# Kernel optimization log

Hardware: AMD Instinct MI355X
Metric: run time of the kernel (lower is better)

## Reference

```python
import jax, jax.numpy as jnp
import numpy as np

N = 50000
E = 800000
IN_DIM = 128
HID = 64
HEADS = 4
NUM_CLASSES = 40
NEG_SLOPE = 0.2
BN_EPS = 1e-5
SM_EPS = 1e-16


def setup_inputs() -> dict:
    key = jax.random.key(0)
    ks = jax.random.split(key, 12)
    d1 = HID * HEADS
    s_in = 1.0 / np.sqrt(IN_DIM)
    s_d1 = 1.0 / np.sqrt(d1)
    return {
        "x": jax.random.normal(ks[0], (N, IN_DIM), dtype=jnp.float32),
        "edge_index": jax.random.randint(ks[1], (2, E), 0, N, dtype=jnp.int32),
        # layer 1 (heads=4, concat)
        "Wl1": jax.random.normal(ks[2], (IN_DIM, d1), dtype=jnp.float32) * s_in,
        "Wr1": jax.random.normal(ks[3], (IN_DIM, d1), dtype=jnp.float32) * s_in,
        "att1": jax.random.normal(ks[4], (HEADS, HID), dtype=jnp.float32) * (1.0 / np.sqrt(HID)),
        "b1": jnp.zeros((d1,), dtype=jnp.float32),
        "gamma1": jnp.ones((d1,), dtype=jnp.float32),
        "beta1": jnp.zeros((d1,), dtype=jnp.float32),
        # layer 2 (heads=1, mean)
        "Wl2": jax.random.normal(ks[5], (d1, NUM_CLASSES), dtype=jnp.float32) * s_d1,
        "Wr2": jax.random.normal(ks[6], (d1, NUM_CLASSES), dtype=jnp.float32) * s_d1,
        "att2": jax.random.normal(ks[7], (1, NUM_CLASSES), dtype=jnp.float32) * (1.0 / np.sqrt(NUM_CLASSES)),
        "b2": jnp.zeros((NUM_CLASSES,), dtype=jnp.float32),
    }


def _gatv2_conv(x, Wl, Wr, att, b, src, dst, heads, out_ch, concat):
    n = x.shape[0]
    xl = (x @ Wl).reshape(n, heads, out_ch)   # source transform
    xr = (x @ Wr).reshape(n, heads, out_ch)   # target transform
    # per-edge attention logits (GATv2): a^T LeakyReLU(xl_j + xr_i)
    s = xl[src] + xr[dst]                                    # [E, H, C]
    e = jnp.einsum('ehc,hc->eh', jax.nn.leaky_relu(s, NEG_SLOPE), att)  # [E, H]
    # segment softmax over incoming edges of each dst node
    m = jax.ops.segment_max(e, dst, num_segments=n)          # [N, H]
    a = jnp.exp(e - m[dst])
    denom = jax.ops.segment_sum(a, dst, num_segments=n)
    alpha = a / (denom[dst] + SM_EPS)                        # [E, H]
    # aggregate messages alpha * xl_j
    out = jax.ops.segment_sum(alpha[..., None] * xl[src], dst, num_segments=n)  # [N, H, C]
    out = out.reshape(n, heads * out_ch) if concat else out.mean(axis=1)
    return out + b


def _batchnorm(h, gamma, beta):
    mu = h.mean(axis=0)
    var = h.var(axis=0)
    return gamma * (h - mu) * jax.lax.rsqrt(var + BN_EPS) + beta


def reference(x, edge_index, Wl1, Wr1, att1, b1, gamma1, beta1, Wl2, Wr2, att2, b2):
    n = x.shape[0]
    # add self-loops (PyG GATv2Conv default add_self_loops=True)
    loop = jnp.arange(n, dtype=edge_index.dtype)
    src = jnp.concatenate([edge_index[0], loop])
    dst = jnp.concatenate([edge_index[1], loop])
    h = _gatv2_conv(x, Wl1, Wr1, att1, b1, src, dst, HEADS, HID, True)
    h = jax.nn.elu(_batchnorm(h, gamma1, beta1))
    # eval mode: dropout is identity
    return _gatv2_conv(h, Wl2, Wr2, att2, b2, src, dst, 1, NUM_CLASSES, False)
```

## Files before the change

kernel.cpp:

```cpp
#include <hip/hip_runtime.h>
#include <math.h>

#define N_NODES 50000
#define N_EDGES 800000
#define ET (N_EDGES + N_NODES)
#define IN_DIM 128
#define HID 64
#define HEADS 4
#define D1 256
#define NCLS 40
#define NEG_SLOPE 0.2f
#define BN_EPS 1e-5f
#define SM_EPS 1e-16f
#define NB 196

typedef unsigned short ushort_t;
typedef __attribute__((ext_vector_type(8))) short short8;
typedef __attribute__((ext_vector_type(16))) float f32x16;

__device__ __forceinline__ float eluf(float x) { return x > 0.f ? x : expm1f(x); }
__device__ __forceinline__ float lrelu(float x) { return x >= 0.f ? x : NEG_SLOPE * x; }
__device__ __forceinline__ unsigned short f2bf(float f) {
    unsigned int u = __float_as_uint(f);
    u += 0x7fffu + ((u >> 16) & 1u);
    return (unsigned short)(u >> 16);
}
__device__ __forceinline__ float bf2f(ushort_t u) {
    return __uint_as_float(((unsigned int)u) << 16);
}

__global__ void k_deg(const int* __restrict__ ei, int* __restrict__ deg) {
    int e = blockIdx.x * blockDim.x + threadIdx.x;
    if (e >= ET) return;
    int dst = (e < N_EDGES) ? ei[N_EDGES + e] : (e - N_EDGES);
    atomicAdd(&deg[dst], 1);
}

__global__ __launch_bounds__(256) void k_scan1(const int* __restrict__ deg,
                                               int* __restrict__ row_st,
                                               int* __restrict__ bsum) {
    __shared__ int wsum[4], woff[4];
    const int t = threadIdx.x, w = t >> 6, lane = t & 63;
    const int idx = blockIdx.x * 256 + t;
    int v = (idx < N_NODES) ? deg[idx] : 0;
    int s = v;
    #pragma unroll
    for (int off = 1; off < 64; off <<= 1) {
        int y = __shfl_up(s, off, 64);
        if (lane >= off) s += y;
    }
    if (lane == 63) wsum[w] = s;
    __syncthreads();
    if (t == 0) {
        int run = 0;
        #pragma unroll
        for (int i2 = 0; i2 < 4; i2++) { woff[i2] = run; run += wsum[i2]; }
        bsum[blockIdx.x] = run;
    }
    __syncthreads();
    if (idx < N_NODES) row_st[idx] = woff[w] + (s - v);
}

__global__ __launch_bounds__(256) void k_scan2(int* __restrict__ bsum) {
    __shared__ int wsum[4], woff[4];
    const int t = threadIdx.x, w = t >> 6, lane = t & 63;
    int v = (t < NB) ? bsum[t] : 0;
    int s = v;
    #pragma unroll
    for (int off = 1; off < 64; off <<= 1) {
        int y = __shfl_up(s, off, 64);
        if (lane >= off) s += y;
    }
    if (lane == 63) wsum[w] = s;
    __syncthreads();
    if (t == 0) {
        int run = 0;
        #pragma unroll
        for (int i2 = 0; i2 < 4; i2++) { woff[i2] = run; run += wsum[i2]; }
    }
    __syncthreads();
    if (t < NB) bsum[t] = woff[w] + (s - v);
}

__global__ void k_scan3(int* __restrict__ row_st, int* __restrict__ cursor,
                        const int* __restrict__ bsum) {
    const int idx = blockIdx.x * 256 + threadIdx.x;
    if (idx < N_NODES) {
        int r = row_st[idx] + bsum[blockIdx.x];
        row_st[idx] = r;
        cursor[idx] = r;
    }
    if (idx == 0) row_st[N_NODES] = ET;
}

__global__ void k_scatter(const int* __restrict__ ei, int* __restrict__ cursor,
                          int* __restrict__ csr_src) {
    int e = blockIdx.x * blockDim.x + threadIdx.x;
    if (e >= ET) return;
    int src, dst;
    if (e < N_EDGES) { src = ei[e]; dst = ei[N_EDGES + e]; }
    else             { src = dst = e - N_EDGES; }
    int pos = atomicAdd(&cursor[dst], 1);
    csr_src[pos] = src;
}

__global__ void k_cvt_x(const float* __restrict__ x, ushort_t* __restrict__ xb, int n4) {
    int i = blockIdx.x * blockDim.x + threadIdx.x;
    if (i >= n4) return;
    float4 v = ((const float4*)x)[i];
    ushort4 o;
    o.x = f2bf(v.x); o.y = f2bf(v.y); o.z = f2bf(v.z); o.w = f2bf(v.w);
    ((ushort4*)xb)[i] = o;
}

__global__ void k_cvt_w1(const float* __restrict__ Wl, const float* __restrict__ Wr,
                         ushort_t* __restrict__ BT) {
    int n = blockIdx.x;
    int k = threadIdx.x;
    float v = (n < 256) ? Wl[k * 256 + n] : Wr[k * 256 + (n - 256)];
    BT[n * 128 + k] = f2bf(v);
}

__global__ void k_cvt_w2(const float* __restrict__ Wl, const float* __restrict__ Wr,
                         ushort_t* __restrict__ BT) {
    int n = blockIdx.x;
    int k = threadIdx.x;
    float v = 0.f;
    if (n < 40)      v = Wl[k * 40 + n];
    else if (n < 80) v = Wr[k * 40 + (n - 40)];
    BT[n * 256 + k] = f2bf(v);
}

__global__ void k_cvt_h(const float* __restrict__ h1, const float* __restrict__ g,
                        const float* __restrict__ b, ushort_t* __restrict__ h1b) {
    int i = blockIdx.x * blockDim.x + threadIdx.x;
    int c0 = (threadIdx.x * 4) & 255;
    float4 v = ((const float4*)h1)[i];
    ushort4 o;
    o.x = f2bf(eluf(g[c0 + 0] * v.x + b[c0 + 0]));
    o.y = f2bf(eluf(g[c0 + 1] * v.y + b[c0 + 1]));
    o.z = f2bf(eluf(g[c0 + 2] * v.z + b[c0 + 2]));
    o.w = f2bf(eluf(g[c0 + 3] * v.w + b[c0 + 3]));
    ((ushort4*)h1b)[i] = o;
}

#define MBM 128
#define MBN 128
#define MBK 64
template<typename OT>
__global__ __launch_bounds__(256) void k_mgemm(
    const ushort_t* __restrict__ A, const ushort_t* __restrict__ BT,
    OT* __restrict__ C, int M, int K, int N, int ldc)
{
    __shared__ __align__(16) ushort_t Al[MBM * MBK];
    __shared__ __align__(16) ushort_t Bl[MBN * MBK];
    const int t = threadIdx.x;
    const int w = t >> 6, L = t & 63;
    const int i0 = blockIdx.x * MBM;
    const int j0 = blockIdx.y * MBN;
    const int wm = (w >> 1) * 64, wn = (w & 1) * 64;
    const int l31 = L & 31, half = L >> 5;

    int sm[4], sca[4];
    #pragma unroll
    for (int r = 0; r < 4; r++) {
        int s = (r * 4 + w) * 64 + L;
        int m = s >> 3;
        sm[r] = m;
        sca[r] = (s & 7) ^ (m & 7);
    }

    f32x16 acc[2][2];
    #pragma unroll
    for (int a = 0; a < 2; a++)
        #pragma unroll
        for (int b = 0; b < 2; b++)
            #pragma unroll
            for (int r = 0; r < 16; r++) acc[a][b][r] = 0.f;

    for (int kt = 0; kt < K; kt += MBK) {
        short8 sa[4], sb[4];
        #pragma unroll
        for (int r = 0; r < 4; r++) {
            int row = i0 + sm[r]; if (row >= M) row = M - 1;
            sa[r] = *(const short8*)&A[(size_t)row * K + kt + sca[r] * 8];
            sb[r] = *(const short8*)&BT[(size_t)(j0 + sm[r]) * K + kt + sca[r] * 8];
        }
        __syncthreads();
        #pragma unroll
        for (int r = 0; r < 4; r++) {
            int s = (r * 4 + w) * 64 + L;
            *(short8*)&Al[s * 8] = sa[r];
            *(short8*)&Bl[s * 8] = sb[r];
        }
        __syncthreads();
        #pragma unroll
        for (int ks = 0; ks < 4; ks++) {
            short8 af[2], bfr[2];
            #pragma unroll
            for (int mt = 0; mt < 2; mt++) {
                int m = wm + mt * 32 + l31;
                int c = (ks * 2 + half) ^ (m & 7);
                af[mt] = *(const short8*)&Al[(m * 8 + c) * 8];
            }
            #pragma unroll
            for (int nt = 0; nt < 2; nt++) {
                int n = wn + nt * 32 + l31;
                int c = (ks * 2 + half) ^ (n & 7);
                bfr[nt] = *(const short8*)&Bl[(n * 8 + c) * 8];
            }
            #pragma unroll
            for (int mt = 0; mt < 2; mt++)
                #pragma unroll
                for (int nt = 0; nt < 2; nt++)
                    acc[mt][nt] = __builtin_amdgcn_mfma_f32_32x32x16_bf16(
                        af[mt], bfr[nt], acc[mt][nt], 0, 0, 0);
        }
    }
    #pragma unroll
    for (int mt = 0; mt < 2; mt++)
        #pragma unroll
        for (int nt = 0; nt < 2; nt++) {
            int col = j0 + wn + nt * 32 + l31;
            int rbase = i0 + wm + mt * 32 + 4 * half;
            if (col < N) {
                #pragma unroll
                for (int r = 0; r < 16; r++) {
                    int row = rbase + (r & 3) + 8 * (r >> 2);
                    if (row < M) {
                        if constexpr (sizeof(OT) == 2)
                            C[(size_t)row * ldc + col] = (OT)f2bf(acc[mt][nt][r]);
                        else
                            C[(size_t)row * ldc + col] = acc[mt][nt][r];
                    }
                }
            }
        }
}

#define CH1 16
#define XLS 260
__global__ __launch_bounds__(256) void k_node1(
    const ushort_t* __restrict__ xlr, const int* __restrict__ row_start,
    const int* __restrict__ csr_src, const float* __restrict__ att1,
    const float* __restrict__ b1, float* __restrict__ h1)
{
    __shared__ __align__(16) float xl_sh[CH1 * XLS];
    __shared__ __align__(16) float xr_sh[D1];
    __shared__ __align__(16) float att_sh[D1];
    __shared__ __align__(16) float p_sh[HEADS][CH1];
    __shared__ int src_sh[CH1];
    const int i = blockIdx.x;
    const int t = threadIdx.x;
    const int h = t >> 6, lane = t & 63;
    const int qe = lane >> 2, qq = lane & 3;
    const int half = lane >> 5, l31 = lane & 31;
    const int s0 = row_start[i], s1 = row_start[i + 1];
    xr_sh[t] = bf2f(xlr[(size_t)i * 512 + 256 + t]);
    att_sh[t] = att1[t];
    const float bvv = b1[t];
    __syncthreads();

    float xr_t[16], at_t[16];
    {
        const float* xrp = &xr_sh[h * 64 + qq * 16];
        const float* atp = &att_sh[h * 64 + qq * 16];
        #pragma unroll
        for (int k = 0; k < 16; k += 4) {
            float4 a = *(const float4*)&xrp[k];
            float4 b = *(const float4*)&atp[k];
            xr_t[k + 0] = a.x; xr_t[k + 1] = a.y; xr_t[k + 2] = a.z; xr_t[k + 3] = a.w;
            at_t[k + 0] = b.x; at_t[k + 1] = b.y; at_t[k + 2] = b.z; at_t[k + 3] = b.w;
        }
    }

    float acc = 0.f, l_run = 0.f;

    int base = s0;
    const int nfull = (s1 - s0) >> 4;
    for (int f = 0; f < nfull; f++, base += CH1) {
        __syncthreads();
        if (t < CH1) src_sh[t] = csr_src[base + t];
        __syncthreads();
        #pragma unroll
        for (int r = 0; r < 2; r++) {
            int e = r * 8 + h * 2 + half;
            const ushort_t* gp = &xlr[(size_t)src_sh[e] * 512];
            ushort4 u0 = *(const ushort4*)&gp[4 * l31];
            ushort4 u1 = *(const ushort4*)&gp[128 + 4 * l31];
            float4 f0 = make_float4(bf2f(u0.x), bf2f(u0.y), bf2f(u0.z), bf2f(u0.w));
            float4 f1 = make_float4(bf2f(u1.x), bf2f(u1.y), bf2f(u1.z), bf2f(u1.w));
            *(float4*)&xl_sh[e * XLS + 4 * l31] = f0;
            *(float4*)&xl_sh[e * XLS + 128 + 4 * l31] = f1;
        }
        __syncthreads();
        float dot = 0.f;
        {
            const float* xp = &xl_sh[qe * XLS + h * 64 + qq * 16];
            #pragma unroll
            for (int k = 0; k < 16; k += 4) {
                float4 v = *(const float4*)&xp[k];
                dot += lrelu(v.x + xr_t[k + 0]) * at_t[k + 0];
                dot += lrelu(v.y + xr_t[k + 1]) * at_t[k + 1];
                dot += lrelu(v.z + xr_t[k + 2]) * at_t[k + 2];
                dot += lrelu(v.w + xr_t[k + 3]) * at_t[k + 3];
            }
        }
        dot += __shfl_xor(dot, 1, 64);
        dot += __shfl_xor(dot, 2, 64);
        if (qq == 0) p_sh[h][qe] = __expf(dot);
        float4 P0 = *(const float4*)&p_sh[h][0];
        float4 P1 = *(const float4*)&p_sh[h][4];
        float4 P2 = *(const float4*)&p_sh[h][8];
        float4 P3 = *(const float4*)&p_sh[h][12];
        float p[16] = {P0.x, P0.y, P0.z, P0.w, P1.x, P1.y, P1.z, P1.w,
                       P2.x, P2.y, P2.z, P2.w, P3.x, P3.y, P3.z, P3.w};
        float lsum = 0.f;
        #pragma unroll
        for (int e = 0; e < 16; e++) lsum += p[e];
        l_run += lsum;
        #pragma unroll
        for (int e = 0; e < 16; e++)
            acc += p[e] * xl_sh[e * XLS + t];
    }
    const int rem = s1 - base;
    if (rem > 0) {
        __syncthreads();
        if (t < rem) src_sh[t] = csr_src[base + t];
        __syncthreads();
        #pragma unroll
        for (int r = 0; r < 2; r++) {
            int e = r * 8 + h * 2 + half;
            if (e < rem) {
                const ushort_t* gp = &xlr[(size_t)src_sh[e] * 512];
                ushort4 u0 = *(const ushort4*)&gp[4 * l31];
                ushort4 u1 = *(const ushort4*)&gp[128 + 4 * l31];
                float4 f0 = make_float4(bf2f(u0.x), bf2f(u0.y), bf2f(u0.z), bf2f(u0.w));
                float4 f1 = make_float4(bf2f(u1.x), bf2f(u1.y), bf2f(u1.z), bf2f(u1.w));
                *(float4*)&xl_sh[e * XLS + 4 * l31] = f0;
                *(float4*)&xl_sh[e * XLS + 128 + 4 * l31] = f1;
            }
        }
        __syncthreads();
        float dot = 0.f;
        {
            const float* xp = &xl_sh[qe * XLS + h * 64 + qq * 16];
            #pragma unroll
            for (int k = 0; k < 16; k += 4) {
                float4 v = *(const float4*)&xp[k];
                dot += lrelu(v.x + xr_t[k + 0]) * at_t[k + 0];
                dot += lrelu(v.y + xr_t[k + 1]) * at_t[k + 1];
                dot += lrelu(v.z + xr_t[k + 2]) * at_t[k + 2];
                dot += lrelu(v.w + xr_t[k + 3]) * at_t[k + 3];
            }
        }
        dot += __shfl_xor(dot, 1, 64);
        dot += __shfl_xor(dot, 2, 64);
        if (qq == 0) p_sh[h][qe] = (qe < rem) ? __expf(dot) : 0.f;
        for (int e = 0; e < rem; e++) {
            float pe = p_sh[h][e];
            l_run += pe;
            acc += pe * xl_sh[e * XLS + t];
        }
    }
    h1[(size_t)i * 256 + t] = acc / (l_run + SM_EPS) + bvv;
}

__global__ void k_bnstats(const float* __restrict__ h1, float* __restrict__ bn_sum,
                          float* __restrict__ bn_sumsq) {
    const int t = threadIdx.x;
    const int rows_per = (N_NODES + gridDim.x - 1) / gridDim.x;
    const int r0 = blockIdx.x * rows_per;
    const int r1 = min(N_NODES, r0 + rows_per);
    float s = 0.f, s2 = 0.f;
    for (int r = r0; r < r1; r++) {
        float v = h1[(size_t)r * 256 + t];
        s += v; s2 += v * v;
    }
    atomicAdd(&bn_sum[t], s);
    atomicAdd(&bn_sumsq[t], s2);
}

__global__ void k_bnfinal(const float* __restrict__ bn_sum, const float* __restrict__ bn_sumsq,
                          const float* __restrict__ gamma, const float* __restrict__ beta,
                          float* __restrict__ bn_g, float* __restrict__ bn_b) {
    const int t = threadIdx.x;
    float mean = bn_sum[t] * (1.f / N_NODES);
    float var = bn_sumsq[t] * (1.f / N_NODES) - mean * mean;
    float g = gamma[t] * rsqrtf(var + BN_EPS);
    bn_g[t] = g;
    bn_b[t] = beta[t] - g * mean;
}

#define C2S 44
__global__ __launch_bounds__(256) void k_node2(
    const ushort_t* __restrict__ xlr2, const int* __restrict__ row_start,
    const int* __restrict__ csr_src, const float* __restrict__ att2,
    const float* __restrict__ b2, float* __restrict__ out)
{
    __shared__ __align__(16) float xl_sh[4][16 * C2S];
    __shared__ __align__(16) float p_sh[4][16];
    __shared__ float xr_blk[4][NCLS];
    __shared__ int src_sh[4][16];
    const int wv = threadIdx.x >> 6, L = threadIdx.x & 63;
    const int i = blockIdx.x * 4 + wv;
    const int qe = L >> 2, qq = L & 3;
    const bool node_ok = (i < N_NODES);
    int s0 = 0, s1 = 0;
    if (node_ok) { s0 = row_start[i]; s1 = row_start[i + 1]; }
    if (node_ok && L < NCLS) xr_blk[wv][L] = bf2f(xlr2[(size_t)i * 80 + 40 + L]);
    float at_t[10], xr_t[10];
    #pragma unroll
    for (int r = 0; r < 10; r++) at_t[r] = att2[qq + 4 * r];
    if (node_ok) {
        #pragma unroll
        for (int r = 0; r < 10; r++) xr_t[r] = xr_blk[wv][qq + 4 * r];
    }

    float accv = 0.f, l_run = 0.f;
    const int cagg = (L < NCLS) ? L : 0;

    if (node_ok)
    for (int base = s0; base < s1; base += 16) {
        const int cnt = min(16, s1 - base);
        if (L < cnt) src_sh[wv][L] = csr_src[base + L];
        {
            int e = L & 15, k = L >> 4;
            float4 f0 = make_float4(0.f, 0.f, 0.f, 0.f), f1 = f0;
            if (e < cnt) {
                short8 u = *(const short8*)&xlr2[(size_t)src_sh[wv][e] * 80 + k * 8];
                f0 = make_float4(bf2f((ushort_t)u[0]), bf2f((ushort_t)u[1]),
                                 bf2f((ushort_t)u[2]), bf2f((ushort_t)u[3]));
                f1 = make_float4(bf2f((ushort_t)u[4]), bf2f((ushort_t)u[5]),
                                 bf2f((ushort_t)u[6]), bf2f((ushort_t)u[7]));
            }
            *(float4*)&xl_sh[wv][e * C2S + k * 8] = f0;
            *(float4*)&xl_sh[wv][e * C2S + k * 8 + 4] = f1;
            if (L < 16) {
                int e2 = L;
                float4 g0 = make_float4(0.f, 0.f, 0.f, 0.f), g1 = g0;
                if (e2 < cnt) {
                    short8 u = *(const short8*)&xlr2[(size_t)src_sh[wv][e2] * 80 + 32];
                    g0 = make_float4(bf2f((ushort_t)u[0]), bf2f((ushort_t)u[1]),
                                     bf2f((ushort_t)u[2]), bf2f((ushort_t)u[3]));
                    g1 = make_float4(bf2f((ushort_t)u[4]), bf2f((ushort_t)u[5]),
                                     bf2f((ushort_t)u[6]), bf2f((ushort_t)u[7]));
                }
                *(float4*)&xl_sh[wv][e2 * C2S + 32] = g0;
                *(float4*)&xl_sh[wv][e2 * C2S + 36] = g1;
            }
        }
        float dot = 0.f;
        #pragma unroll
        for (int r = 0; r < 10; r++) {
            float v = xl_sh[wv][qe * C2S + qq + 4 * r];
            dot += lrelu(v + xr_t[r]) * at_t[r];
        }
        dot += __shfl_xor(dot, 1, 64);
        dot += __shfl_xor(dot, 2, 64);
        if (qq == 0) p_sh[wv][qe] = (qe < cnt) ? __expf(dot) : 0.f;
        float4 P0 = *(const float4*)&p_sh[wv][0];
        float4 P1 = *(const float4*)&p_sh[wv][4];
        float4 P2 = *(const float4*)&p_sh[wv][8];
        float4 P3 = *(const float4*)&p_sh[wv][12];
        float p[16] = {P0.x, P0.y, P0.z, P0.w, P1.x, P1.y, P1.z, P1.w,
                       P2.x, P2.y, P2.z, P2.w, P3.x, P3.y, P3.z, P3.w};
        float lsum = 0.f;
        #pragma unroll
        for (int e = 0; e < 16; e++) lsum += p[e];
        l_run += lsum;
        #pragma unroll
        for (int e = 0; e < 16; e++)
            accv += p[e] * xl_sh[wv][e * C2S + cagg];
    }
    if (node_ok && L < NCLS)
        out[(size_t)i * 40 + L] = accv / (l_run + SM_EPS) + b2[L];
}

static inline size_t align_up(size_t v, size_t a) { return (v + a - 1) & ~(a - 1); }

extern "C" void kernel_launch(void* const* d_in, const int* in_sizes, int n_in,
                              void* d_out, int out_size, void* d_ws, size_t ws_size,
                              hipStream_t stream)
{
    const float* x     = (const float*)d_in[0];
    const int*   ei    = (const int*)d_in[1];
    const float* Wl1   = (const float*)d_in[2];
    const float* Wr1   = (const float*)d_in[3];
    const float* att1  = (const float*)d_in[4];
    const float* b1    = (const float*)d_in[5];
    const float* gamma1= (const float*)d_in[6];
    const float* beta1 = (const float*)d_in[7];
    const float* Wl2   = (const float*)d_in[8];
    const float* Wr2   = (const float*)d_in[9];
    const float* att2  = (const float*)d_in[10];
    const float* b2    = (const float*)d_in[11];
    float* out = (float*)d_out;

    char* ws = (char*)d_ws;
    size_t off = 0;
    ushort_t* xlr1b = (ushort_t*)(ws + off); off += (size_t)N_NODES * 512 * 2;
    float*    h1    = (float*)   (ws + off); off += (size_t)N_NODES * 256 * 4;
    ushort_t* h1b   = (ushort_t*)(ws + off); off += (size_t)N_NODES * 256 * 2;
    int*   csr_src = (int*)  (ws + off); off += align_up((size_t)ET * 4, 256);
    int*   row_st  = (int*)  (ws + off); off += align_up((size_t)(N_NODES + 1) * 4, 256);
    int*   cursor  = (int*)  (ws + off); off += align_up((size_t)N_NODES * 4, 256);
    int*   deg     = (int*)  (ws + off); off += align_up((size_t)N_NODES * 4, 256);
    int*   bsum    = (int*)  (ws + off); off += align_up((size_t)NB * 4, 256);
    float* bn_sum  = (float*)(ws + off); off += 256 * 4;
    float* bn_sumsq= (float*)(ws + off); off += 256 * 4;
    float* bn_g    = (float*)(ws + off); off += 256 * 4;
    float* bn_b    = (float*)(ws + off); off += 256 * 4;
    ushort_t* BT1  = (ushort_t*)(ws + off); off += align_up((size_t)512 * 128 * 2, 256);
    ushort_t* BT2  = (ushort_t*)(ws + off); off += align_up((size_t)128 * 256 * 2, 256);
    ushort_t* xlr2b = xlr1b;
    ushort_t* xb    = (ushort_t*)h1;

    hipMemsetAsync(deg, 0, (size_t)N_NODES * 4, stream);
    hipMemsetAsync(bn_sum, 0, 512 * 4, stream);

    k_deg<<<(ET + 255) / 256, 256, 0, stream>>>(ei, deg);
    k_scan1<<<NB, 256, 0, stream>>>(deg, row_st, bsum);
    k_scan2<<<1, 256, 0, stream>>>(bsum);
    k_scan3<<<NB, 256, 0, stream>>>(row_st, cursor, bsum);
    k_scatter<<<(ET + 255) / 256, 256, 0, stream>>>(ei, cursor, csr_src);

    k_cvt_x<<<(N_NODES * IN_DIM / 4 + 255) / 256, 256, 0, stream>>>(x, xb, N_NODES * IN_DIM / 4);
    k_cvt_w1<<<512, 128, 0, stream>>>(Wl1, Wr1, BT1);
    k_cvt_w2<<<128, 256, 0, stream>>>(Wl2, Wr2, BT2);

    dim3 g1((N_NODES + MBM - 1) / MBM, 512 / MBN);
    k_mgemm<ushort_t><<<g1, 256, 0, stream>>>(xb, BT1, xlr1b, N_NODES, IN_DIM, 512, 512);
    k_node1<<<N_NODES, 256, 0, stream>>>(xlr1b, row_st, csr_src, att1, b1, h1);

    k_bnstats<<<250, 256, 0, stream>>>(h1, bn_sum, bn_sumsq);
    k_bnfinal<<<1, 256, 0, stream>>>(bn_sum, bn_sumsq, gamma1, beta1, bn_g, bn_b);
    k_cvt_h<<<(N_NODES * 256 / 4 + 255) / 256, 256, 0, stream>>>(h1, bn_g, bn_b, h1b);

    dim3 g2((N_NODES + MBM - 1) / MBM, 1);
    k_mgemm<ushort_t><<<g2, 256, 0, stream>>>(h1b, BT2, xlr2b, N_NODES, D1, 80, 80);
    k_node2<<<(N_NODES + 3) / 4, 256, 0, stream>>>(xlr2b, row_st, csr_src, att2, b2, out);
}
```

Measured before the change: 490.3 us.

## Fuse BN+ELU conversion into layer-2 GEMM and trim node-kernel syncs

```diff
diff --git a/kernel.cpp b/kernel.cpp
--- a/kernel.cpp
+++ b/kernel.cpp
@@ -129,19 +129,6 @@
     if (n < 40)      v = Wl[k * 40 + n];
     else if (n < 80) v = Wr[k * 40 + (n - 40)];
     BT[n * 256 + k] = f2bf(v);
-}
-
-__global__ void k_cvt_h(const float* __restrict__ h1, const float* __restrict__ g,
-                        const float* __restrict__ b, ushort_t* __restrict__ h1b) {
-    int i = blockIdx.x * blockDim.x + threadIdx.x;
-    int c0 = (threadIdx.x * 4) & 255;
-    float4 v = ((const float4*)h1)[i];
-    ushort4 o;
-    o.x = f2bf(eluf(g[c0 + 0] * v.x + b[c0 + 0]));
-    o.y = f2bf(eluf(g[c0 + 1] * v.y + b[c0 + 1]));
-    o.z = f2bf(eluf(g[c0 + 2] * v.z + b[c0 + 2]));
-    o.w = f2bf(eluf(g[c0 + 3] * v.w + b[c0 + 3]));
-    ((ushort4*)h1b)[i] = o;
 }
 
 #define MBM 128
@@ -238,6 +225,112 @@
         }
 }
 
+__global__ __launch_bounds__(256) void k_mgemm_bn(
+    const float* __restrict__ A, const ushort_t* __restrict__ BT,
+    ushort_t* __restrict__ C, int M, int K, int N, int ldc,
+    const float* __restrict__ bn_g, const float* __restrict__ bn_b)
+{
+    __shared__ __align__(16) ushort_t Al[MBM * MBK];
+    __shared__ __align__(16) ushort_t Bl[MBN * MBK];
+    __shared__ float gsh[256], bsh[256];
+    const int t = threadIdx.x;
+    const int w = t >> 6, L = t & 63;
+    const int i0 = blockIdx.x * MBM;
+    const int j0 = blockIdx.y * MBN;
+    const int wm = (w >> 1) * 64, wn = (w & 1) * 64;
+    const int l31 = L & 31, half = L >> 5;
+    gsh[t] = bn_g[t]; bsh[t] = bn_b[t];
+    __syncthreads();
+
+    int sm[4], sca[4];
+    #pragma unroll
+    for (int r = 0; r < 4; r++) {
+        int s = (r * 4 + w) * 64 + L;
+        int m = s >> 3;
+        sm[r] = m;
+        sca[r] = (s & 7) ^ (m & 7);
+    }
+
+    f32x16 acc[2][2];
+    #pragma unroll
+    for (int a = 0; a < 2; a++)
+        #pragma unroll
+        for (int b = 0; b < 2; b++)
+            #pragma unroll
+            for (int r = 0; r < 16; r++) acc[a][b][r] = 0.f;
+
+    for (int kt = 0; kt < K; kt += MBK) {
+        short8 sa[4], sb[4];
+        #pragma unroll
+        for (int r = 0; r < 4; r++) {
+            int row = i0 + sm[r]; if (row >= M) row = M - 1;
+            int kb = kt + sca[r] * 8;
+            float4 v0 = *(const float4*)&A[(size_t)row * K + kb];
+            float4 v1 = *(const float4*)&A[(size_t)row * K + kb + 4];
+            float4 g0 = *(const float4*)&gsh[kb];
+            float4 g1 = *(const float4*)&gsh[kb + 4];
+            float4 b0 = *(const float4*)&bsh[kb];
+            float4 b1v = *(const float4*)&bsh[kb + 4];
+            short8 o;
+            o[0] = (short)f2bf(eluf(g0.x * v0.x + b0.x));
+            o[1] = (short)f2bf(eluf(g0.y * v0.y + b0.y));
+            o[2] = (short)f2bf(eluf(g0.z * v0.z + b0.z));
+            o[3] = (short)f2bf(eluf(g0.w * v0.w + b0.w));
+            o[4] = (short)f2bf(eluf(g1.x * v1.x + b1v.x));
+            o[5] = (short)f2bf(eluf(g1.y * v1.y + b1v.y));
+            o[6] = (short)f2bf(eluf(g1.z * v1.z + b1v.z));
+            o[7] = (short)f2bf(eluf(g1.w * v1.w + b1v.w));
+            sa[r] = o;
+            sb[r] = *(const short8*)&BT[(size_t)(j0 + sm[r]) * K + kb];
+        }
+        __syncthreads();
+        #pragma unroll
+        for (int r = 0; r < 4; r++) {
+            int s = (r * 4 + w) * 64 + L;
+            *(short8*)&Al[s * 8] = sa[r];
+            *(short8*)&Bl[s * 8] = sb[r];
+        }
+        __syncthreads();
+        #pragma unroll
+        for (int ks = 0; ks < 4; ks++) {
+            short8 af[2], bfr[2];
+            #pragma unroll
+            for (int mt = 0; mt < 2; mt++) {
+                int m = wm + mt * 32 + l31;
+                int c = (ks * 2 + half) ^ (m & 7);
+                af[mt] = *(const short8*)&Al[(m * 8 + c) * 8];
+            }
+            #pragma unroll
+            for (int nt = 0; nt < 2; nt++) {
+                int n = wn + nt * 32 + l31;
+                int c = (ks * 2 + half) ^ (n & 7);
+                bfr[nt] = *(const short8*)&Bl[(n * 8 + c) * 8];
+            }
+            #pragma unroll
+            for (int mt = 0; mt < 2; mt++)
+                #pragma unroll
+                for (int nt = 0; nt < 2; nt++)
+                    acc[mt][nt] = __builtin_amdgcn_mfma_f32_32x32x16_bf16(
+                        af[mt], bfr[nt], acc[mt][nt], 0, 0, 0);
+        }
+    }
+    #pragma unroll
+    for (int mt = 0; mt < 2; mt++)
+        #pragma unroll
+        for (int nt = 0; nt < 2; nt++) {
+            int col = j0 + wn + nt * 32 + l31;
+            int rbase = i0 + wm + mt * 32 + 4 * half;
+            if (col < N) {
+                #pragma unroll
+                for (int r = 0; r < 16; r++) {
+                    int row = rbase + (r & 3) + 8 * (r >> 2);
+                    if (row < M)
+                        C[(size_t)row * ldc + col] = f2bf(acc[mt][nt][r]);
+                }
+            }
+        }
+}
+
 #define CH1 16
 #define XLS 260
 __global__ __launch_bounds__(256) void k_node1(
@@ -246,33 +339,28 @@
     const float* __restrict__ b1, float* __restrict__ h1)
 {
     __shared__ __align__(16) float xl_sh[CH1 * XLS];
-    __shared__ __align__(16) float xr_sh[D1];
-    __shared__ __align__(16) float att_sh[D1];
     __shared__ __align__(16) float p_sh[HEADS][CH1];
-    __shared__ int src_sh[CH1];
     const int i = blockIdx.x;
     const int t = threadIdx.x;
     const int h = t >> 6, lane = t & 63;
     const int qe = lane >> 2, qq = lane & 3;
     const int half = lane >> 5, l31 = lane & 31;
     const int s0 = row_start[i], s1 = row_start[i + 1];
-    xr_sh[t] = bf2f(xlr[(size_t)i * 512 + 256 + t]);
-    att_sh[t] = att1[t];
-    const float bvv = b1[t];
-    __syncthreads();
 
     float xr_t[16], at_t[16];
     {
-        const float* xrp = &xr_sh[h * 64 + qq * 16];
-        const float* atp = &att_sh[h * 64 + qq * 16];
+        const ushort_t* xrp = &xlr[(size_t)i * 512 + 256 + h * 64 + qq * 16];
+        const float* atp = &att1[h * 64 + qq * 16];
         #pragma unroll
         for (int k = 0; k < 16; k += 4) {
-            float4 a = *(const float4*)&xrp[k];
+            ushort4 u = *(const ushort4*)&xrp[k];
             float4 b = *(const float4*)&atp[k];
-            xr_t[k + 0] = a.x; xr_t[k + 1] = a.y; xr_t[k + 2] = a.z; xr_t[k + 3] = a.w;
+            xr_t[k + 0] = bf2f(u.x); xr_t[k + 1] = bf2f(u.y);
+            xr_t[k + 2] = bf2f(u.z); xr_t[k + 3] = bf2f(u.w);
             at_t[k + 0] = b.x; at_t[k + 1] = b.y; at_t[k + 2] = b.z; at_t[k + 3] = b.w;
         }
     }
+    const float bvv = b1[t];
 
     float acc = 0.f, l_run = 0.f;
 
@@ -280,12 +368,11 @@
     const int nfull = (s1 - s0) >> 4;
     for (int f = 0; f < nfull; f++, base += CH1) {
         __syncthreads();
-        if (t < CH1) src_sh[t] = csr_src[base + t];
-        __syncthreads();
         #pragma unroll
         for (int r = 0; r < 2; r++) {
             int e = r * 8 + h * 2 + half;
-            const ushort_t* gp = &xlr[(size_t)src_sh[e] * 512];
+            int src = csr_src[base + e];
+            const ushort_t* gp = &xlr[(size_t)src * 512];
             ushort4 u0 = *(const ushort4*)&gp[4 * l31];
             ushort4 u1 = *(const ushort4*)&gp[128 + 4 * l31];
             float4 f0 = make_float4(bf2f(u0.x), bf2f(u0.y), bf2f(u0.z), bf2f(u0.w));
@@ -326,13 +413,12 @@
     const int rem = s1 - base;
     if (rem > 0) {
         __syncthreads();
-        if (t < rem) src_sh[t] = csr_src[base + t];
-        __syncthreads();
         #pragma unroll
         for (int r = 0; r < 2; r++) {
             int e = r * 8 + h * 2 + half;
             if (e < rem) {
-                const ushort_t* gp = &xlr[(size_t)src_sh[e] * 512];
+                int src = csr_src[base + e];
+                const ushort_t* gp = &xlr[(size_t)src * 512];
                 ushort4 u0 = *(const ushort4*)&gp[4 * l31];
                 ushort4 u1 = *(const ushort4*)&gp[128 + 4 * l31];
                 float4 f0 = make_float4(bf2f(u0.x), bf2f(u0.y), bf2f(u0.z), bf2f(u0.w));
@@ -400,7 +486,6 @@
 {
     __shared__ __align__(16) float xl_sh[4][16 * C2S];
     __shared__ __align__(16) float p_sh[4][16];
-    __shared__ float xr_blk[4][NCLS];
     __shared__ int src_sh[4][16];
     const int wv = threadIdx.x >> 6, L = threadIdx.x & 63;
     const int i = blockIdx.x * 4 + wv;
@@ -408,70 +493,101 @@
     const bool node_ok = (i < N_NODES);
     int s0 = 0, s1 = 0;
     if (node_ok) { s0 = row_start[i]; s1 = row_start[i + 1]; }
-    if (node_ok && L < NCLS) xr_blk[wv][L] = bf2f(xlr2[(size_t)i * 80 + 40 + L]);
     float at_t[10], xr_t[10];
     #pragma unroll
     for (int r = 0; r < 10; r++) at_t[r] = att2[qq + 4 * r];
     if (node_ok) {
-        #pragma unroll
-        for (int r = 0; r < 10; r++) xr_t[r] = xr_blk[wv][qq + 4 * r];
+        const ushort_t* xrp = &xlr2[(size_t)i * 80 + 40];
+        #pragma unroll
+        for (int r = 0; r < 10; r++) xr_t[r] = bf2f(xrp[qq + 4 * r]);
     }
 
     float accv = 0.f, l_run = 0.f;
     const int cagg = (L < NCLS) ? L : 0;
-
-    if (node_ok)
-    for (int base = s0; base < s1; base += 16) {
-        const int cnt = min(16, s1 - base);
-        if (L < cnt) src_sh[wv][L] = csr_src[base + L];
-        {
-            int e = L & 15, k = L >> 4;
-            float4 f0 = make_float4(0.f, 0.f, 0.f, 0.f), f1 = f0;
-            if (e < cnt) {
-                short8 u = *(const short8*)&xlr2[(size_t)src_sh[wv][e] * 80 + k * 8];
-                f0 = make_float4(bf2f((ushort_t)u[0]), bf2f((ushort_t)u[1]),
-                                 bf2f((ushort_t)u[2]), bf2f((ushort_t)u[3]));
-                f1 = make_float4(bf2f((ushort_t)u[4]), bf2f((ushort_t)u[5]),
-                                 bf2f((ushort_t)u[6]), bf2f((ushort_t)u[7]));
-            }
-            *(float4*)&xl_sh[wv][e * C2S + k * 8] = f0;
-            *(float4*)&xl_sh[wv][e * C2S + k * 8 + 4] = f1;
-            if (L < 16) {
-                int e2 = L;
-                float4 g0 = make_float4(0.f, 0.f, 0.f, 0.f), g1 = g0;
-                if (e2 < cnt) {
-                    short8 u = *(const short8*)&xlr2[(size_t)src_sh[wv][e2] * 80 + 32];
-                    g0 = make_float4(bf2f((ushort_t)u[0]), bf2f((ushort_t)u[1]),
-                                     bf2f((ushort_t)u[2]), bf2f((ushort_t)u[3]));
-                    g1 = make_float4(bf2f((ushort_t)u[4]), bf2f((ushort_t)u[5]),
-                                     bf2f((ushort_t)u[6]), bf2f((ushort_t)u[7]));
+    const int e16 = L & 15, k16 = L >> 4;
+
+    if (node_ok) {
+        int base = s0;
+        const int nfull = (s1 - s0) >> 4;
+        for (int f = 0; f < nfull; f++, base += 16) {
+            if (L < 16) src_sh[wv][L] = csr_src[base + L];
+            {
+                short8 u = *(const short8*)&xlr2[(size_t)src_sh[wv][e16] * 80 + k16 * 8];
+                float4 f0 = make_float4(bf2f((ushort_t)u[0]), bf2f((ushort_t)u[1]),
+                                        bf2f((ushort_t)u[2]), bf2f((ushort_t)u[3]));
+                float4 f1 = make_float4(bf2f((ushort_t)u[4]), bf2f((ushort_t)u[5]),
+                                        bf2f((ushort_t)u[6]), bf2f((ushort_t)u[7]));
+                *(float4*)&xl_sh[wv][e16 * C2S + k16 * 8] = f0;
+                *(float4*)&xl_sh[wv][e16 * C2S + k16 * 8 + 4] = f1;
+                if (L < 16) {
+                    short8 u2 = *(const short8*)&xlr2[(size_t)src_sh[wv][L] * 80 + 32];
+                    float4 g0 = make_float4(bf2f((ushort_t)u2[0]), bf2f((ushort_t)u2[1]),
+                                            bf2f((ushort_t)u2[2]), bf2f((ushort_t)u2[3]));
+                    float4 g1 = make_float4(bf2f((ushort_t)u2[4]), bf2f((ushort_t)u2[5]),
+                                            bf2f((ushort_t)u2[6]), bf2f((ushort_t)u2[7]));
+                    *(float4*)&xl_sh[wv][L * C2S + 32] = g0;
+                    *(float4*)&xl_sh[wv][L * C2S + 36] = g1;
                 }
-                *(float4*)&xl_sh[wv][e2 * C2S + 32] = g0;
-                *(float4*)&xl_sh[wv][e2 * C2S + 36] = g1;
-            }
-        }
-        float dot = 0.f;
-        #pragma unroll
-        for (int r = 0; r < 10; r++) {
-            float v = xl_sh[wv][qe * C2S + qq + 4 * r];
-            dot += lrelu(v + xr_t[r]) * at_t[r];
-        }
-        dot += __shfl_xor(dot, 1, 64);
-        dot += __shfl_xor(dot, 2, 64);
-        if (qq == 0) p_sh[wv][qe] = (qe < cnt) ? __expf(dot) : 0.f;
-        float4 P0 = *(const float4*)&p_sh[wv][0];
-        float4 P1 = *(const float4*)&p_sh[wv][4];
-        float4 P2 = *(const float4*)&p_sh[wv][8];
-        float4 P3 = *(const float4*)&p_sh[wv][12];
-        float p[16] = {P0.x, P0.y, P0.z, P0.w, P1.x, P1.y, P1.z, P1.w,
-                       P2.x, P2.y, P2.z, P2.w, P3.x, P3.y, P3.z, P3.w};
-        float lsum = 0.f;
-        #pragma unroll
-        for (int e = 0; e < 16; e++) lsum += p[e];
-        l_run += lsum;
-        #pragma unroll
-        for (int e = 0; e < 16; e++)
-            accv += p[e] * xl_sh[wv][e * C2S + cagg];
+            }
+            float dot = 0.f;
+            #pragma unroll
+            for (int r = 0; r < 10; r++) {
+                float v = xl_sh[wv][qe * C2S + qq + 4 * r];
+                dot += lrelu(v + xr_t[r]) * at_t[r];
+            }
+            dot += __shfl_xor(dot, 1, 64);
+            dot += __shfl_xor(dot, 2, 64);
+            if (qq == 0) p_sh[wv][qe] = __expf(dot);
+            float4 P0 = *(const float4*)&p_sh[wv][0];
+            float4 P1 = *(const float4*)&p_sh[wv][4];
+            float4 P2 = *(const float4*)&p_sh[wv][8];
+            float4 P3 = *(const float4*)&p_sh[wv][12];
+            float p[16] = {P0.x, P0.y, P0.z, P0.w, P1.x, P1.y, P1.z, P1.w,
+                           P2.x, P2.y, P2.z, P2.w, P3.x, P3.y, P3.z, P3.w};
+            float lsum = 0.f;
+            #pragma unroll
+            for (int e = 0; e < 16; e++) lsum += p[e];
+            l_run += lsum;
+            #pragma unroll
+            for (int e = 0; e < 16; e++)
+                accv += p[e] * xl_sh[wv][e * C2S + cagg];
+        }
+        const int rem = s1 - base;
+        if (rem > 0) {
+            if (L < rem) src_sh[wv][L] = csr_src[base + L];
+            if (e16 < rem) {
+                short8 u = *(const short8*)&xlr2[(size_t)src_sh[wv][e16] * 80 + k16 * 8];
+                float4 f0 = make_float4(bf2f((ushort_t)u[0]), bf2f((ushort_t)u[1]),
+                                        bf2f((ushort_t)u[2]), bf2f((ushort_t)u[3]));
+                float4 f1 = make_float4(bf2f((ushort_t)u[4]), bf2f((ushort_t)u[5]),
+                                        bf2f((ushort_t)u[6]), bf2f((ushort_t)u[7]));
+                *(float4*)&xl_sh[wv][e16 * C2S + k16 * 8] = f0;
+                *(float4*)&xl_sh[wv][e16 * C2S + k16 * 8 + 4] = f1;
+            }
+            if (L < rem) {
+                short8 u2 = *(const short8*)&xlr2[(size_t)src_sh[wv][L] * 80 + 32];
+                float4 g0 = make_float4(bf2f((ushort_t)u2[0]), bf2f((ushort_t)u2[1]),
+                                        bf2f((ushort_t)u2[2]), bf2f((ushort_t)u2[3]));
+                float4 g1 = make_float4(bf2f((ushort_t)u2[4]), bf2f((ushort_t)u2[5]),
+                                        bf2f((ushort_t)u2[6]), bf2f((ushort_t)u2[7]));
+                *(float4*)&xl_sh[wv][L * C2S + 32] = g0;
+                *(float4*)&xl_sh[wv][L * C2S + 36] = g1;
+            }
+            float dot = 0.f;
+            #pragma unroll
+            for (int r = 0; r < 10; r++) {
+                float v = xl_sh[wv][qe * C2S + qq + 4 * r];
+                dot += lrelu(v + xr_t[r]) * at_t[r];
+            }
+            dot += __shfl_xor(dot, 1, 64);
+            dot += __shfl_xor(dot, 2, 64);
+            if (qq == 0) p_sh[wv][qe] = (qe < rem) ? __expf(dot) : 0.f;
+            for (int e = 0; e < rem; e++) {
+                float pe = p_sh[wv][e];
+                l_run += pe;
+                accv += pe * xl_sh[wv][e * C2S + cagg];
+            }
+        }
     }
     if (node_ok && L < NCLS)
         out[(size_t)i * 40 + L] = accv / (l_run + SM_EPS) + b2[L];
@@ -501,7 +617,6 @@
     size_t off = 0;
     ushort_t* xlr1b = (ushort_t*)(ws + off); off += (size_t)N_NODES * 512 * 2;
     float*    h1    = (float*)   (ws + off); off += (size_t)N_NODES * 256 * 4;
-    ushort_t* h1b   = (ushort_t*)(ws + off); off += (size_t)N_NODES * 256 * 2;
     int*   csr_src = (int*)  (ws + off); off += align_up((size_t)ET * 4, 256);
     int*   row_st  = (int*)  (ws + off); off += align_up((size_t)(N_NODES + 1) * 4, 256);
     int*   cursor  = (int*)  (ws + off); off += align_up((size_t)N_NODES * 4, 256);
@@ -533,11 +648,10 @@
     k_mgemm<ushort_t><<<g1, 256, 0, stream>>>(xb, BT1, xlr1b, N_NODES, IN_DIM, 512, 512);
     k_node1<<<N_NODES, 256, 0, stream>>>(xlr1b, row_st, csr_src, att1, b1, h1);
 
-    k_bnstats<<<250, 256, 0, stream>>>(h1, bn_sum, bn_sumsq);
+    k_bnstats<<<1000, 256, 0, stream>>>(h1, bn_sum, bn_sumsq);
     k_bnfinal<<<1, 256, 0, stream>>>(bn_sum, bn_sumsq, gamma1, beta1, bn_g, bn_b);
-    k_cvt_h<<<(N_NODES * 256 / 4 + 255) / 256, 256, 0, stream>>>(h1, bn_g, bn_b, h1b);
 
     dim3 g2((N_NODES + MBM - 1) / MBM, 1);
-    k_mgemm<ushort_t><<<g2, 256, 0, stream>>>(h1b, BT2, xlr2b, N_NODES, D1, 80, 80);
+    k_mgemm_bn<<<g2, 256, 0, stream>>>(h1, BT2, xlr2b, N_NODES, D1, 80, 80, bn_g, bn_b);
     k_node2<<<(N_NODES + 3) / 4, 256, 0, stream>>>(xlr2b, row_st, csr_src, att2, b2, out);
 }
```

Result: faster. 468.4 us (-4.5%).
